# Kernel tuning notes

Measured on AMD Instinct MI355X. Metric: run time of the kernel, lower is better.

The kernel has to match this reference:

```python
import jax, jax.numpy as jnp
import numpy as np

N_NODES = 50000
N_EDGES = 800000
IN, HID, OUT = 512, 256, 128


def spmm(edge_src, edge_dst, edge_weight, x, n_nodes):
    # y[i] = sum_{e: dst[e]==i} w[e] * x[src[e]]   (sparse adjacency @ x)
    msgs = edge_weight[:, None] * x[edge_src]          # [E, F] gather
    return jax.ops.segment_sum(msgs, edge_dst, num_segments=n_nodes)


def setup_inputs() -> dict:
    key = jax.random.key(0)
    k1, k2, k3, k4, k5, k6 = jax.random.split(key, 6)
    features = jax.random.normal(k1, (N_NODES, IN), dtype=jnp.float32)
    edge_src = jax.random.randint(k2, (N_EDGES,), 0, N_NODES, dtype=jnp.int32)
    edge_dst = jax.random.randint(k3, (N_EDGES,), 0, N_NODES, dtype=jnp.int32)
    edge_weight = jax.random.uniform(k4, (N_EDGES,), dtype=jnp.float32)
    # init like torch: uniform(-stdv, stdv), stdv = 1/sqrt(out_dim)
    s1 = 1.0 / np.sqrt(HID)
    s2 = 1.0 / np.sqrt(OUT)
    W1 = jax.random.uniform(k5, (IN, HID), dtype=jnp.float32, minval=-s1, maxval=s1)
    W2 = jax.random.uniform(k6, (HID, OUT), dtype=jnp.float32, minval=-s2, maxval=s2)
    return {"features": features, "edge_src": edge_src, "edge_dst": edge_dst,
            "edge_weight": edge_weight, "W1": W1, "W2": W2}


def reference(features, edge_src, edge_dst, edge_weight, W1, W2):
    n = features.shape[0]
    # layer 1: dense GEMM -> SpMM -> ReLU
    hidden = jax.nn.relu(spmm(edge_src, edge_dst, edge_weight, features @ W1, n))
    # layer 2: dense GEMM -> SpMM
    out = spmm(edge_src, edge_dst, edge_weight, hidden @ W2, n)
    return out
```

## Files before the change

kernel.cpp:

```cpp
#include <hip/hip_runtime.h>

#define NN 50000
#define NE 800000
#define FIN 512
#define FHID 256
#define FOUT 128
#define MPAD 50048

#define CAST_BLOCKS 12500
#define TW1_BLOCKS  512
#define TW2_BLOCKS  128

#define NBKT   196
#define BCAP   5120
#define BSTRIDE 16
#define PA_BLOCKS 392
#define E_CHA    2048

#define PB_BLOCKS   196
#define GEMM1_BLOCKS 782

using bf16x8 = __attribute__((ext_vector_type(8))) short;
using f32x4  = __attribute__((ext_vector_type(4))) float;
using u16x8  = __attribute__((ext_vector_type(8))) unsigned short;
using u16x4  = __attribute__((ext_vector_type(4))) unsigned short;
using u16x2  = __attribute__((ext_vector_type(2))) unsigned short;

__device__ __forceinline__ unsigned short f2bf(float f) {
    unsigned int u = __builtin_bit_cast(unsigned int, f);
    unsigned int r = (u + 0x7FFFu + ((u >> 16) & 1u)) >> 16;
    return (unsigned short)r;
}
__device__ __forceinline__ float bf2f(unsigned short u) {
    return __builtin_bit_cast(float, (unsigned int)u << 16);
}
__device__ __forceinline__ void gload_lds16(const void* g, void* l) {
    __builtin_amdgcn_global_load_lds(
        (const __attribute__((address_space(1))) void*)g,
        (__attribute__((address_space(3))) void*)l, 16, 0, 0);
}


__device__ __forceinline__ void passa_body(int pa,
                                           const int* __restrict__ src,
                                           const int* __restrict__ dst,
                                           const float* __restrict__ w,
                                           int* __restrict__ bcur,
                                           int2* __restrict__ barr) {
    __shared__ int hist[NBKT];
    __shared__ int resv[NBKT];
    int tid = threadIdx.x;
    if (tid < NBKT) hist[tid] = 0;
    __syncthreads();
    int base = pa * E_CHA + tid;
    int  d[8];
    bool m[8];
#pragma unroll
    for (int j = 0; j < 8; ++j) {
        int e = base + j * 256;
        m[j] = e < NE;
        d[j] = m[j] ? dst[e] : 0;
    }
#pragma unroll
    for (int j = 0; j < 8; ++j)
        if (m[j]) atomicAdd(&hist[d[j] >> 8], 1);
    __syncthreads();
    if (tid < NBKT) {
        int h = hist[tid];
        resv[tid] = (h > 0) ? atomicAdd(&bcur[tid * BSTRIDE], h) : 0;
        hist[tid] = 0;
    }
    __syncthreads();
    int   s[8];
    float wv[8];
#pragma unroll
    for (int j = 0; j < 8; ++j) {
        int e = base + j * 256;
        s[j]  = m[j] ? src[e] : 0;
        wv[j] = m[j] ? w[e] : 0.f;
    }
#pragma unroll
    for (int j = 0; j < 8; ++j) {
        if (m[j]) {
            int bb = d[j] >> 8;
            int r  = atomicAdd(&hist[bb], 1);
            int pos = resv[bb] + r;
            if (pos < BCAP)
                barr[(size_t)bb * BCAP + pos] =
                    make_int2(s[j] | ((d[j] & 255) << 16), __float_as_int(wv[j]));
        }
    }
}


__global__ __launch_bounds__(256) void fused_pre_kernel(
    const float* __restrict__ X, unsigned short* __restrict__ Xb,
    const int* __restrict__ src, const int* __restrict__ dst,
    const float* __restrict__ w,
    int* __restrict__ bcur, int2* __restrict__ barr,
    const float* __restrict__ W1, unsigned short* __restrict__ W1T,
    const float* __restrict__ W2, unsigned short* __restrict__ W2T) {
    int b = blockIdx.x, tid = threadIdx.x;
    if (b < PA_BLOCKS) {
        passa_body(b, src, dst, w, bcur, barr);
    } else if (b < PA_BLOCKS + CAST_BLOCKS) {
        int i = (b - PA_BLOCKS) * 512 + tid;
        const float4* p = (const float4*)X;
        float4 a = p[i], c = p[i + 256];
        u16x4 va, vc;
        va[0] = f2bf(a.x); va[1] = f2bf(a.y); va[2] = f2bf(a.z); va[3] = f2bf(a.w);
        vc[0] = f2bf(c.x); vc[1] = f2bf(c.y); vc[2] = f2bf(c.z); vc[3] = f2bf(c.w);
        ((u16x4*)Xb)[i]       = va;
        ((u16x4*)Xb)[i + 256] = vc;
    } else if (b < PA_BLOCKS + CAST_BLOCKS + TW1_BLOCKS) {
        int t = (b - PA_BLOCKS - CAST_BLOCKS) * 256 + tid;
        int n = t % FHID, k = t / FHID;
        W1T[(size_t)n * FIN + k] = f2bf(W1[t]);
    } else {
        int t = (b - PA_BLOCKS - CAST_BLOCKS - TW1_BLOCKS) * 256 + tid;
        int n = t % FOUT, k = t / FOUT;
        W2T[(size_t)n * FHID + k] = f2bf(W2[t]);
    }
}


__global__ __launch_bounds__(256) void scan_bkt_kernel(const int* __restrict__ bcur,
                                                       int* __restrict__ bko,
                                                       int* __restrict__ off) {
    __shared__ int wsum[4];
    int tid = threadIdx.x, lane = tid & 63, wid = tid >> 6;
    int v = (tid < NBKT) ? min(bcur[tid * BSTRIDE], BCAP) : 0;
    int s = v;
#pragma unroll
    for (int d = 1; d < 64; d <<= 1) {
        int t = __shfl_up(s, d, 64);
        if (lane >= d) s += t;
    }
    if (lane == 63) wsum[wid] = s;
    __syncthreads();
    int wo = 0;
#pragma unroll
    for (int j = 0; j < 4; ++j)
        if (j < wid) wo += wsum[j];
    int excl = wo + s - v;
    if (tid < NBKT) bko[tid] = excl;
    if (tid == NBKT - 1) off[NN] = excl + v;
}


template <int K, int N>
__device__ __forceinline__ void gemm_body(const unsigned short* __restrict__ A,
                                          const unsigned short* __restrict__ BT,
                                          unsigned short* __restrict__ C,
                                          int M, int bx, int by) {
    __shared__ unsigned short As[128 * 64];
    __shared__ unsigned short Bs[128 * 64];

    const int tid  = threadIdx.x;
    const int lane = tid & 63;
    const int wid  = tid >> 6;
    const int wm   = wid >> 1;
    const int wn   = wid & 1;
    const int brow = bx * 128;
    const int bcol = by * 128;
    const int r15   = lane & 15;
    const int khalf = (lane >> 4) * 8;

    f32x4 acc[4][4] = {};

    for (int k0 = 0; k0 < K; k0 += 64) {
#pragma unroll
        for (int c = 0; c < 4; ++c) {
            int b   = wid * 4096 + c * 1024 + lane * 16;
            int row = b >> 7;
            int cby = (b & 127) ^ ((row & 7) << 4);
            const char* ga = (const char*)(A + (size_t)(brow + row) * K + k0) + cby;
            gload_lds16(ga, (char*)As + wid * 4096 + c * 1024);
            const char* gb = (const char*)(BT + (size_t)(bcol + row) * K + k0) + cby;
            gload_lds16(gb, (char*)Bs + wid * 4096 + c * 1024);
        }
        __syncthreads();

        bf16x8 af[4][2], bfr[4][2];
#pragma unroll
        for (int m = 0; m < 4; ++m) {
            int row = wm * 64 + m * 16 + r15;
            int rb  = row * 128;
            int sw  = (row & 7) << 4;
#pragma unroll
            for (int ks = 0; ks < 2; ++ks) {
                int byte = rb + (((ks * 32 + khalf) * 2) ^ sw);
                af[m][ks] = *(const bf16x8*)((const char*)As + byte);
            }
        }
#pragma unroll
        for (int n = 0; n < 4; ++n) {
            int row = wn * 64 + n * 16 + r15;
            int rb  = row * 128;
            int sw  = (row & 7) << 4;
#pragma unroll
            for (int ks = 0; ks < 2; ++ks) {
                int byte = rb + (((ks * 32 + khalf) * 2) ^ sw);
                bfr[n][ks] = *(const bf16x8*)((const char*)Bs + byte);
            }
        }
#pragma unroll
        for (int m = 0; m < 4; ++m)
#pragma unroll
            for (int n = 0; n < 4; ++n)
#pragma unroll
                for (int ks = 0; ks < 2; ++ks)
                    acc[m][n] = __builtin_amdgcn_mfma_f32_16x16x32_bf16(
                        af[m][ks], bfr[n][ks], acc[m][n], 0, 0, 0);
        __syncthreads();
    }

    const int crow0 = brow + wm * 64;
    const int ccol0 = bcol + wn * 64 + r15;
    const int rsub  = (lane >> 4) * 4;
#pragma unroll
    for (int m = 0; m < 4; ++m) {
#pragma unroll
        for (int r = 0; r < 4; ++r) {
            int grow = crow0 + m * 16 + rsub + r;
            if (grow < M) {
#pragma unroll
                for (int n = 0; n < 4; ++n)
                    C[(size_t)grow * N + ccol0 + n * 16] = f2bf(acc[m][n][r]);
            }
        }
    }
}


__device__ __forceinline__ void passb_body(int b, const int2* __restrict__ barr,
                                           const int* __restrict__ bcur,
                                           const int* __restrict__ bko,
                                           int* __restrict__ off,
                                           int2* __restrict__ csr) {
    __shared__ int cnt[256];
    __shared__ int pre[256];
    __shared__ int wsum[4];
    int tid = threadIdx.x, lane = tid & 63, wid = tid >> 6;
    int total = min(bcur[b * BSTRIDE], BCAP);
    int bko_b = bko[b];
    const int2* seg = barr + (size_t)b * BCAP;

    cnt[tid] = 0;
    __syncthreads();
    for (int k = tid; k < total; k += 256)
        atomicAdd(&cnt[(seg[k].x >> 16) & 255], 1);
    __syncthreads();
    int v = cnt[tid];
    int s = v;
#pragma unroll
    for (int d = 1; d < 64; d <<= 1) {
        int t = __shfl_up(s, d, 64);
        if (lane >= d) s += t;
    }
    if (lane == 63) wsum[wid] = s;
    __syncthreads();
    int wo = 0;
#pragma unroll
    for (int j = 0; j < 4; ++j)
        if (j < wid) wo += wsum[j];
    int base = bko_b + wo + s - v;
    pre[tid] = base;
    int n = b * 256 + tid;
    if (n < NN) off[n] = base;
    cnt[tid] = 0;
    __syncthreads();
    for (int k = tid; k < total; k += 256) {
        int2 pl = seg[k];
        int dlow = (pl.x >> 16) & 255;
        int r = atomicAdd(&cnt[dlow], 1);
        csr[pre[dlow] + r] = make_int2(pl.x & 0xFFFF, pl.y);
    }
}


__global__ __launch_bounds__(256) void fused_gemm1_finalize_kernel(
    const unsigned short* __restrict__ A, const unsigned short* __restrict__ BT,
    unsigned short* __restrict__ C,
    const int2* __restrict__ barr, const int* __restrict__ bcur,
    const int* __restrict__ bko, int* __restrict__ off, int2* __restrict__ csr) {
    if (blockIdx.x < PB_BLOCKS) {
        passb_body(blockIdx.x, barr, bcur, bko, off, csr);
    } else {
        int g = blockIdx.x - PB_BLOCKS;
        gemm_body<FIN, FHID>(A, BT, C, NN, g % 391, g / 391);
    }
}

template <int K, int N>
__global__ __launch_bounds__(256) void gemm_bf16_kernel(const unsigned short* __restrict__ A,
                                                        const unsigned short* __restrict__ BT,
                                                        unsigned short* __restrict__ C,
                                                        int M) {
    gemm_body<K, N>(A, BT, C, M, blockIdx.x, blockIdx.y);
}


__global__ __launch_bounds__(256) void spmm_pair_kernel(const unsigned short* __restrict__ X,
                                                        const int* __restrict__ off,
                                                        const int2* __restrict__ csr,
                                                        unsigned short* __restrict__ Y) {
    int wave = (int)((blockIdx.x * 256 + threadIdx.x) >> 6);
    int lane = threadIdx.x & 63;
    int half = lane >> 5;
    int hl   = lane & 31;
    int n = wave * 2 + half;
    if (n >= NN) return;
    int e0 = off[n];
    int e1 = off[n + 1];
    const size_t fo = (size_t)hl * 8;

    float acc[8] = {};
    for (int e = e0; e < e1; e += 8) {
        int   ss[8];
        float ww[8];
#pragma unroll
        for (int j = 0; j < 8; ++j) {
            int  ee = e + j;
            bool v  = ee < e1;
            int2 sw = csr[v ? ee : e0];
            ss[j] = sw.x;
            ww[j] = v ? __int_as_float(sw.y) : 0.f;
        }
        u16x8 r[8];
#pragma unroll
        for (int j = 0; j < 8; ++j)
            r[j] = *(const u16x8*)(X + (size_t)ss[j] * FHID + fo);
#pragma unroll
        for (int j = 0; j < 8; ++j)
#pragma unroll
            for (int k = 0; k < 8; ++k)
                acc[k] += ww[j] * bf2f(r[j][k]);
    }
    u16x8 o;
#pragma unroll
    for (int k = 0; k < 8; ++k) o[k] = f2bf(fmaxf(acc[k], 0.f));
    *(u16x8*)(Y + (size_t)n * FHID + fo) = o;
}


__global__ __launch_bounds__(256) void spmm_quad_kernel(const unsigned short* __restrict__ X,
                                                        const int* __restrict__ off,
                                                        const int2* __restrict__ csr,
                                                        float* __restrict__ Y) {
    int wave = (int)((blockIdx.x * 256 + threadIdx.x) >> 6);
    int lane = threadIdx.x & 63;
    int q  = lane >> 4;
    int hl = lane & 15;
    int n = wave * 4 + q;
    if (n >= NN) return;
    int e0 = off[n];
    int e1 = off[n + 1];
    const size_t fo = (size_t)hl * 8;

    float acc[8] = {};
    for (int e = e0; e < e1; e += 8) {
        int   ss[8];
        float ww[8];
#pragma unroll
        for (int j = 0; j < 8; ++j) {
            int  ee = e + j;
            bool v  = ee < e1;
            int2 sw = csr[v ? ee : e0];
            ss[j] = sw.x;
            ww[j] = v ? __int_as_float(sw.y) : 0.f;
        }
        u16x8 r[8];
#pragma unroll
        for (int j = 0; j < 8; ++j)
            r[j] = *(const u16x8*)(X + (size_t)ss[j] * FOUT + fo);
#pragma unroll
        for (int j = 0; j < 8; ++j)
#pragma unroll
            for (int k = 0; k < 8; ++k)
                acc[k] += ww[j] * bf2f(r[j][k]);
    }
    float4 o0 = make_float4(acc[0], acc[1], acc[2], acc[3]);
    float4 o1 = make_float4(acc[4], acc[5], acc[6], acc[7]);
    *(float4*)(Y + (size_t)n * FOUT + fo) = o0;
    *(float4*)(Y + (size_t)n * FOUT + fo + 4) = o1;
}


extern "C" void kernel_launch(void* const* d_in, const int* in_sizes, int n_in,
                              void* d_out, int out_size, void* d_ws, size_t ws_size,
                              hipStream_t stream) {
    const float* features = (const float*)d_in[0];
    const int*   edge_src = (const int*)d_in[1];
    const int*   edge_dst = (const int*)d_in[2];
    const float* edge_w   = (const float*)d_in[3];
    const float* W1       = (const float*)d_in[4];
    const float* W2       = (const float*)d_in[5];
    float* out = (float*)d_out;

    char*  ws  = (char*)d_ws;
    size_t ofs = 0;
    auto carve = [&](size_t bytes) -> void* {
        void* r = ws + ofs;
        ofs = (ofs + bytes + 255) & ~(size_t)255;
        return r;
    };
    int*            off   = (int*)carve((NN + 1) * sizeof(int));
    int*            bcur  = (int*)carve(NBKT * BSTRIDE * sizeof(int));
    int*            bko   = (int*)carve(NBKT * sizeof(int));
    int2*           barr  = (int2*)carve((size_t)NBKT * BCAP * sizeof(int2));
    int2*           csr   = (int2*)carve((size_t)NE * sizeof(int2));
    unsigned short* Xb    = (unsigned short*)carve((size_t)MPAD * FIN * 2);
    unsigned short* W1T   = (unsigned short*)carve((size_t)FHID * FIN * 2);
    unsigned short* W2T   = (unsigned short*)carve((size_t)FOUT * FHID * 2);
    unsigned short* H0b   = (unsigned short*)carve((size_t)MPAD * FHID * 2);
    unsigned short* Hb    = (unsigned short*)carve((size_t)MPAD * FHID * 2);
    unsigned short* H1b   = H0b;

    hipMemsetAsync(bcur, 0, NBKT * BSTRIDE * sizeof(int), stream);

    fused_pre_kernel<<<PA_BLOCKS + CAST_BLOCKS + TW1_BLOCKS + TW2_BLOCKS, 256, 0, stream>>>(
        features, Xb, edge_src, edge_dst, edge_w, bcur, barr, W1, W1T, W2, W2T);

    scan_bkt_kernel<<<1, 256, 0, stream>>>(bcur, bko, off);

    fused_gemm1_finalize_kernel<<<PB_BLOCKS + GEMM1_BLOCKS, 256, 0, stream>>>(
        Xb, W1T, H0b, barr, bcur, bko, off, csr);

    spmm_pair_kernel<<<6250, 256, 0, stream>>>(H0b, off, csr, Hb);

    gemm_bf16_kernel<FHID, FOUT><<<dim3(391, 1), 256, 0, stream>>>(Hb, W2T, H1b, NN);
    spmm_quad_kernel<<<3125, 256, 0, stream>>>(H1b, off, csr, out);
}
```

Measured before the change: 176.0 us.

## Fuse fp32-to-bf16 feature cast into GEMM1 A-tile loading

Removes the separate pass that cast the 50000x512 fp32 feature matrix to bf16. GEMM1 now reads fp32 rows directly, converts them in registers and stores swizzled bf16 into LDS, while B still uses direct global-to-LDS loads. The memset of the bucket counters moves into a new prep kernel, and pass A gets its own kernel launch. This saves a full write and re-read of the bf16 copy, but A loads become synchronous register loads at twice the byte width, and it adds one kernel launch.

```diff
diff --git a/kernel.cpp b/kernel.cpp
--- a/kernel.cpp
+++ b/kernel.cpp
@@ -7,9 +7,9 @@
 #define FOUT 128
 #define MPAD 50048
 
-#define CAST_BLOCKS 12500
 #define TW1_BLOCKS  512
 #define TW2_BLOCKS  128
+#define ZERO_BLOCKS 13
 
 #define NBKT   196
 #define BCAP   5120
@@ -41,15 +41,34 @@
 }
 
 
-__device__ __forceinline__ void passa_body(int pa,
-                                           const int* __restrict__ src,
-                                           const int* __restrict__ dst,
-                                           const float* __restrict__ w,
-                                           int* __restrict__ bcur,
-                                           int2* __restrict__ barr) {
+__global__ __launch_bounds__(256) void prep_kernel(
+    int* __restrict__ bcur,
+    const float* __restrict__ W1, unsigned short* __restrict__ W1T,
+    const float* __restrict__ W2, unsigned short* __restrict__ W2T) {
+    int b = blockIdx.x, tid = threadIdx.x;
+    if (b < TW1_BLOCKS) {
+        int t = b * 256 + tid;
+        int n = t % FHID, k = t / FHID;
+        W1T[(size_t)n * FIN + k] = f2bf(W1[t]);
+    } else if (b < TW1_BLOCKS + TW2_BLOCKS) {
+        int t = (b - TW1_BLOCKS) * 256 + tid;
+        int n = t % FOUT, k = t / FOUT;
+        W2T[(size_t)n * FHID + k] = f2bf(W2[t]);
+    } else {
+        int i = (b - TW1_BLOCKS - TW2_BLOCKS) * 256 + tid;
+        if (i < NBKT * BSTRIDE) bcur[i] = 0;
+    }
+}
+
+
+__global__ __launch_bounds__(256) void passa_kernel(const int* __restrict__ src,
+                                                    const int* __restrict__ dst,
+                                                    const float* __restrict__ w,
+                                                    int* __restrict__ bcur,
+                                                    int2* __restrict__ barr) {
     __shared__ int hist[NBKT];
     __shared__ int resv[NBKT];
-    int tid = threadIdx.x;
+    int pa = blockIdx.x, tid = threadIdx.x;
     if (tid < NBKT) hist[tid] = 0;
     __syncthreads();
     int base = pa * E_CHA + tid;
@@ -93,37 +112,6 @@
 }
 
 
-__global__ __launch_bounds__(256) void fused_pre_kernel(
-    const float* __restrict__ X, unsigned short* __restrict__ Xb,
-    const int* __restrict__ src, const int* __restrict__ dst,
-    const float* __restrict__ w,
-    int* __restrict__ bcur, int2* __restrict__ barr,
-    const float* __restrict__ W1, unsigned short* __restrict__ W1T,
-    const float* __restrict__ W2, unsigned short* __restrict__ W2T) {
-    int b = blockIdx.x, tid = threadIdx.x;
-    if (b < PA_BLOCKS) {
-        passa_body(b, src, dst, w, bcur, barr);
-    } else if (b < PA_BLOCKS + CAST_BLOCKS) {
-        int i = (b - PA_BLOCKS) * 512 + tid;
-        const float4* p = (const float4*)X;
-        float4 a = p[i], c = p[i + 256];
-        u16x4 va, vc;
-        va[0] = f2bf(a.x); va[1] = f2bf(a.y); va[2] = f2bf(a.z); va[3] = f2bf(a.w);
-        vc[0] = f2bf(c.x); vc[1] = f2bf(c.y); vc[2] = f2bf(c.z); vc[3] = f2bf(c.w);
-        ((u16x4*)Xb)[i]       = va;
-        ((u16x4*)Xb)[i + 256] = vc;
-    } else if (b < PA_BLOCKS + CAST_BLOCKS + TW1_BLOCKS) {
-        int t = (b - PA_BLOCKS - CAST_BLOCKS) * 256 + tid;
-        int n = t % FHID, k = t / FHID;
-        W1T[(size_t)n * FIN + k] = f2bf(W1[t]);
-    } else {
-        int t = (b - PA_BLOCKS - CAST_BLOCKS - TW1_BLOCKS) * 256 + tid;
-        int n = t % FOUT, k = t / FOUT;
-        W2T[(size_t)n * FHID + k] = f2bf(W2[t]);
-    }
-}
-
-
 __global__ __launch_bounds__(256) void scan_bkt_kernel(const int* __restrict__ bcur,
                                                        int* __restrict__ bko,
                                                        int* __restrict__ off) {
@@ -145,6 +133,105 @@
     int excl = wo + s - v;
     if (tid < NBKT) bko[tid] = excl;
     if (tid == NBKT - 1) off[NN] = excl + v;
+}
+
+
+__device__ __forceinline__ void gemm1_body(const float* __restrict__ X,
+                                           const unsigned short* __restrict__ BT,
+                                           unsigned short* __restrict__ C,
+                                           int bx, int by) {
+    __shared__ unsigned short As[128 * 64];
+    __shared__ unsigned short Bs[128 * 64];
+
+    const int tid  = threadIdx.x;
+    const int lane = tid & 63;
+    const int wid  = tid >> 6;
+    const int wm   = wid >> 1;
+    const int wn   = wid & 1;
+    const int brow = bx * 128;
+    const int bcol = by * 128;
+    const int r15   = lane & 15;
+    const int khalf = (lane >> 4) * 8;
+
+    f32x4 acc[4][4] = {};
+
+    for (int k0 = 0; k0 < FIN; k0 += 64) {
+#pragma unroll
+        for (int c = 0; c < 4; ++c) {
+            int b   = wid * 4096 + c * 1024 + lane * 16;
+            int row = b >> 7;
+            int cby = (b & 127) ^ ((row & 7) << 4);
+            const char* gb = (const char*)(BT + (size_t)(bcol + row) * FIN + k0) + cby;
+            gload_lds16(gb, (char*)Bs + wid * 4096 + c * 1024);
+        }
+#pragma unroll
+        for (int g = 0; g < 4; ++g) {
+            int idx  = g * 256 + tid;
+            int row  = idx >> 3;
+            int col0 = (idx & 7) * 8;
+            float4 a0 = make_float4(0.f, 0.f, 0.f, 0.f), a1 = a0;
+            int grow = brow + row;
+            if (grow < NN) {
+                const float4* p = (const float4*)(X + (size_t)grow * FIN + k0 + col0);
+                a0 = p[0]; a1 = p[1];
+            }
+            u16x8 v;
+            v[0] = f2bf(a0.x); v[1] = f2bf(a0.y); v[2] = f2bf(a0.z); v[3] = f2bf(a0.w);
+            v[4] = f2bf(a1.x); v[5] = f2bf(a1.y); v[6] = f2bf(a1.z); v[7] = f2bf(a1.w);
+            int byte = row * 128 + ((col0 * 2) ^ ((row & 7) << 4));
+            *(u16x8*)((char*)As + byte) = v;
+        }
+        __syncthreads();
+
+        bf16x8 af[4][2], bfr[4][2];
+#pragma unroll
+        for (int m = 0; m < 4; ++m) {
+            int row = wm * 64 + m * 16 + r15;
+            int rb  = row * 128;
+            int sw  = (row & 7) << 4;
+#pragma unroll
+            for (int ks = 0; ks < 2; ++ks) {
+                int byte = rb + (((ks * 32 + khalf) * 2) ^ sw);
+                af[m][ks] = *(const bf16x8*)((const char*)As + byte);
+            }
+        }
+#pragma unroll
+        for (int n = 0; n < 4; ++n) {
+            int row = wn * 64 + n * 16 + r15;
+            int rb  = row * 128;
+            int sw  = (row & 7) << 4;
+#pragma unroll
+            for (int ks = 0; ks < 2; ++ks) {
+                int byte = rb + (((ks * 32 + khalf) * 2) ^ sw);
+                bfr[n][ks] = *(const bf16x8*)((const char*)Bs + byte);
+            }
+        }
+#pragma unroll
+        for (int m = 0; m < 4; ++m)
+#pragma unroll
+            for (int n = 0; n < 4; ++n)
+#pragma unroll
+                for (int ks = 0; ks < 2; ++ks)
+                    acc[m][n] = __builtin_amdgcn_mfma_f32_16x16x32_bf16(
+                        af[m][ks], bfr[n][ks], acc[m][n], 0, 0, 0);
+        __syncthreads();
+    }
+
+    const int crow0 = brow + wm * 64;
+    const int ccol0 = bcol + wn * 64 + r15;
+    const int rsub  = (lane >> 4) * 4;
+#pragma unroll
+    for (int m = 0; m < 4; ++m) {
+#pragma unroll
+        for (int r = 0; r < 4; ++r) {
+            int grow = crow0 + m * 16 + rsub + r;
+            if (grow < NN) {
+#pragma unroll
+                for (int n = 0; n < 4; ++n)
+                    C[(size_t)grow * FHID + ccol0 + n * 16] = f2bf(acc[m][n][r]);
+            }
+        }
+    }
 }
 
 
@@ -280,7 +367,7 @@
 
 
 __global__ __launch_bounds__(256) void fused_gemm1_finalize_kernel(
-    const unsigned short* __restrict__ A, const unsigned short* __restrict__ BT,
+    const float* __restrict__ X, const unsigned short* __restrict__ BT,
     unsigned short* __restrict__ C,
     const int2* __restrict__ barr, const int* __restrict__ bcur,
     const int* __restrict__ bko, int* __restrict__ off, int2* __restrict__ csr) {
@@ -288,7 +375,7 @@
         passb_body(blockIdx.x, barr, bcur, bko, off, csr);
     } else {
         int g = blockIdx.x - PB_BLOCKS;
-        gemm_body<FIN, FHID>(A, BT, C, NN, g % 391, g / 391);
+        gemm1_body(X, BT, C, g % 391, g / 391);
     }
 }
 
@@ -410,22 +497,21 @@
     int*            bko   = (int*)carve(NBKT * sizeof(int));
     int2*           barr  = (int2*)carve((size_t)NBKT * BCAP * sizeof(int2));
     int2*           csr   = (int2*)carve((size_t)NE * sizeof(int2));
-    unsigned short* Xb    = (unsigned short*)carve((size_t)MPAD * FIN * 2);
     unsigned short* W1T   = (unsigned short*)carve((size_t)FHID * FIN * 2);
     unsigned short* W2T   = (unsigned short*)carve((size_t)FOUT * FHID * 2);
     unsigned short* H0b   = (unsigned short*)carve((size_t)MPAD * FHID * 2);
     unsigned short* Hb    = (unsigned short*)carve((size_t)MPAD * FHID * 2);
     unsigned short* H1b   = H0b;
 
-    hipMemsetAsync(bcur, 0, NBKT * BSTRIDE * sizeof(int), stream);
-
-    fused_pre_kernel<<<PA_BLOCKS + CAST_BLOCKS + TW1_BLOCKS + TW2_BLOCKS, 256, 0, stream>>>(
-        features, Xb, edge_src, edge_dst, edge_w, bcur, barr, W1, W1T, W2, W2T);
+    prep_kernel<<<TW1_BLOCKS + TW2_BLOCKS + ZERO_BLOCKS, 256, 0, stream>>>(
+        bcur, W1, W1T, W2, W2T);
+
+    passa_kernel<<<PA_BLOCKS, 256, 0, stream>>>(edge_src, edge_dst, edge_w, bcur, barr);
 
     scan_bkt_kernel<<<1, 256, 0, stream>>>(bcur, bko, off);
 
     fused_gemm1_finalize_kernel<<<PB_BLOCKS + GEMM1_BLOCKS, 256, 0, stream>>>(
-        Xb, W1T, H0b, barr, bcur, bko, off, csr);
+        features, W1T, H0b, barr, bcur, bko, off, csr);
 
     spmm_pair_kernel<<<6250, 256, 0, stream>>>(H0b, off, csr, Hb);
 
```

Measured after the change: 175.4 us. About the same (-0.3%).
